# Optimization experiments

Measured on AMD Instinct MI355X. Metric: run time of the kernel, lower is better.

Reference implementation:

```python
import jax, jax.numpy as jnp
import numpy as np

N = 50000        # nodes
E = 200000       # edges
D_IN = 128       # dim_input
D_E = 32         # dim_edge_features
D_H = 256        # dim_hidden
D_OUT = 256      # dim_output
N_LAYERS = 3
N_FRAG = 10000
N_GRAPH = 2000
BN_EPS = 1e-5
GINE_EPS = 0.0   # eps buffer, train_eps=False

_LAYER_DIMS = [(D_IN, D_H), (D_H, D_H), (D_H, D_OUT)]  # (node in, node out) per layer


def setup_inputs() -> dict:
    key = jax.random.key(0)
    ks = iter(jax.random.split(key, 64))
    inp = {}
    inp['x'] = jax.random.normal(next(ks), (N, D_IN), dtype=jnp.float32)
    inp['edge_attr'] = jax.random.normal(next(ks), (E, D_E), dtype=jnp.float32)
    inp['edge_index'] = jax.random.randint(next(ks), (2, E), 0, N, dtype=jnp.int64)
    inp['frag_batch'] = jnp.sort(jax.random.randint(next(ks), (N,), 0, N_FRAG, dtype=jnp.int64))
    inp['graph_batch'] = jnp.sort(jax.random.randint(next(ks), (N,), 0, N_GRAPH, dtype=jnp.int64))
    for i, (din, dout) in enumerate(_LAYER_DIMS):
        fin = din + D_E  # MLP input = node feat + edge feat (post-concat message)
        inp[f'w1_{i}'] = jax.random.normal(next(ks), (fin, D_H), dtype=jnp.float32) / np.sqrt(fin)
        inp[f'b1_{i}'] = jnp.zeros((D_H,), dtype=jnp.float32)
        inp[f'w2_{i}'] = jax.random.normal(next(ks), (D_H, dout), dtype=jnp.float32) / np.sqrt(D_H)
        inp[f'b2_{i}'] = jnp.zeros((dout,), dtype=jnp.float32)
        inp[f'g_{i}'] = jnp.ones((dout,), dtype=jnp.float32)     # BN weight
        inp[f'beta_{i}'] = jnp.zeros((dout,), dtype=jnp.float32)  # BN bias
    return inp


def _gine_layer(x, edge_attr, src, dst, w1, b1, w2, b2, g, beta):
    # message: relu(concat(x_j, e_ji)) gathered along edges  -> [E, din+De]
    m = jax.nn.relu(jnp.concatenate([x[src], edge_attr], axis=-1))
    # aggregate: scatter-add into target nodes -> [N, din+De]
    agg = jax.ops.segment_sum(m, dst, num_segments=N)
    # (1+eps)*x residual on the node-feature slice
    agg = agg.at[:, : x.shape[1]].add((1.0 + GINE_EPS) * x)
    # h_Theta MLP: Linear -> ReLU -> Linear
    h = jnp.dot(jax.nn.relu(jnp.dot(agg, w1) + b1), w2) + b2
    # ReLU then BatchNorm1d(track_running_stats=False): batch stats, biased var
    h = jax.nn.relu(h)
    mu = h.mean(axis=0)
    var = h.var(axis=0)
    return g * (h - mu) * jax.lax.rsqrt(var + BN_EPS) + beta


def _sqrt_pool(h, batch, num_segments):
    # nodes_per_graph, broadcast back per-node, sqrt-normalize, then add-pool
    cnt = jax.ops.segment_sum(jnp.ones((h.shape[0],), h.dtype), batch, num_segments=num_segments)
    inv_sqrt = jax.lax.rsqrt(jnp.maximum(cnt, 1.0))[batch]  # [N]
    return jax.ops.segment_sum(h * inv_sqrt[:, None], batch, num_segments=num_segments)


def reference(x, edge_attr, edge_index, frag_batch, graph_batch,
              w1_0, b1_0, w2_0, b2_0, g_0, beta_0,
              w1_1, b1_1, w2_1, b2_1, g_1, beta_1,
              w1_2, b1_2, w2_2, b2_2, g_2, beta_2):
    src, dst = edge_index[0], edge_index[1]
    params = [(w1_0, b1_0, w2_0, b2_0, g_0, beta_0),
              (w1_1, b1_1, w2_1, b2_1, g_1, beta_1),
              (w1_2, b1_2, w2_2, b2_2, g_2, beta_2)]
    h = x
    for p in params:
        h = _gine_layer(h, edge_attr, src, dst, *p)
    frag_out = _sqrt_pool(h, frag_batch, N_FRAG)    # [N_FRAG, D_OUT]
    graph_out = _sqrt_pool(h, graph_batch, N_GRAPH)  # [N_GRAPH, D_OUT]
    return (frag_out, graph_out)
```

## Files before the change

### kernel.cpp

```cpp
#include <hip/hip_runtime.h>

#define N_NODES 50000
#define N_EDGES 200000
#define DE 32
#define N_FRAG 10000
#define N_GRAPH 2000
#define BN_SLOTS 32
#define KSTR 296

typedef _Float16 f16x8 __attribute__((ext_vector_type(8)));
typedef _Float16 f16x4 __attribute__((ext_vector_type(4)));
typedef __attribute__((ext_vector_type(4))) float f32x4;

__device__ __forceinline__ float4 ld4(const float* p) { return *(const float4*)p; }
__device__ __forceinline__ float4 ld4(const _Float16* p) {
    f16x4 h = *(const f16x4*)p;
    float4 v; v.x = (float)h[0]; v.y = (float)h[1]; v.z = (float)h[2]; v.w = (float)h[3];
    return v;
}
__device__ __forceinline__ void st4h(_Float16* p, float4 v) {
    f16x4 h = {(_Float16)v.x, (_Float16)v.y, (_Float16)v.z, (_Float16)v.w};
    *(f16x4*)p = h;
}

__global__ __launch_bounds__(256)
void count_deg_kernel(const int* __restrict__ ei, int* __restrict__ deg) {
    int e = blockIdx.x * 256 + threadIdx.x;
    if (e < N_EDGES) atomicAdd(&deg[ei[N_EDGES + e]], 1);
}

__global__ __launch_bounds__(256)
void block_sum_kernel(const int* __restrict__ deg, int* __restrict__ bsum) {
    int i = blockIdx.x * 256 + threadIdx.x;
    int v = (i < N_NODES) ? deg[i] : 0;
#pragma unroll
    for (int o = 1; o < 64; o <<= 1) v += __shfl_xor(v, o);
    __shared__ int wsum[4];
    if ((threadIdx.x & 63) == 0) wsum[threadIdx.x >> 6] = v;
    __syncthreads();
    if (threadIdx.x == 0) bsum[blockIdx.x] = wsum[0] + wsum[1] + wsum[2] + wsum[3];
}

__global__ __launch_bounds__(256)
void top_scan_kernel(int* __restrict__ bsum, int nb) {
    __shared__ int s[256];
    int t = threadIdx.x;
    s[t] = (t < nb) ? bsum[t] : 0;
    __syncthreads();
    for (int o = 1; o < 256; o <<= 1) {
        int v = s[t];
        int a = (t >= o) ? s[t - o] : 0;
        __syncthreads();
        s[t] = v + a;
        __syncthreads();
    }
    if (t < nb) bsum[t] = (t > 0) ? s[t - 1] : 0;
}

__global__ __launch_bounds__(256)
void final_scan_kernel(const int* __restrict__ deg, const int* __restrict__ bsum,
                       int* __restrict__ ptr) {
    __shared__ int s[256];
    int i = blockIdx.x * 256 + threadIdx.x;
    int t = threadIdx.x;
    int v = (i < N_NODES) ? deg[i] : 0;
    s[t] = v;
    __syncthreads();
    for (int o = 1; o < 256; o <<= 1) {
        int x = s[t];
        int a = (t >= o) ? s[t - o] : 0;
        __syncthreads();
        s[t] = x + a;
        __syncthreads();
    }
    int incl = s[t];
    int base = bsum[blockIdx.x];
    if (i < N_NODES) ptr[i] = base + incl - v;
    if (i == N_NODES - 1) ptr[N_NODES] = base + incl;
}

__global__ __launch_bounds__(256)
void fill_csr_kernel(const int* __restrict__ ei, const int* __restrict__ row_ptr,
                     int* __restrict__ fill, int* __restrict__ csr_src,
                     int* __restrict__ csr_eid) {
    int e = blockIdx.x * 256 + threadIdx.x;
    if (e >= N_EDGES) return;
    int dst = ei[N_EDGES + e];
    int pos = row_ptr[dst] + atomicAdd(&fill[dst], 1);
    csr_src[pos] = ei[e];
    csr_eid[pos] = e;
}

__global__ __launch_bounds__(256)
void segptr2_kernel(const int* __restrict__ fb, const int* __restrict__ gb,
                    int* __restrict__ frag_ptr, int* __restrict__ graph_ptr) {
    int id = blockIdx.x * 256 + threadIdx.x;
    const int* batch;
    int* ptr;
    int s;
    if (id <= N_FRAG) { batch = fb; ptr = frag_ptr; s = id; }
    else if (id <= N_FRAG + 1 + N_GRAPH) { batch = gb; ptr = graph_ptr; s = id - (N_FRAG + 1); }
    else return;
    int lo = 0, hi = N_NODES;
    while (lo < hi) {
        int mid = (lo + hi) >> 1;
        if (batch[mid] < s) lo = mid + 1; else hi = mid;
    }
    ptr[s] = lo;
}

struct BsAll {
    const float* W[6];
    _Float16* BS[6];
    int base[7];
};

__global__ __launch_bounds__(256)
void bs16_all_kernel(BsAll a) {
    int id = blockIdx.x * 256 + threadIdx.x;
    if (id >= a.base[6]) return;
    int seg = 0;
#pragma unroll
    for (int i = 1; i < 6; ++i) seg += (id >= a.base[i]);
    int lid = id - a.base[seg];
    int j  = lid & 7;
    int l  = (lid >> 3) & 63;
    int cg = (lid >> 9) & 15;
    int kt = lid >> 13;
    int col = cg * 16 + (l & 15);
    int k   = kt * 32 + (l >> 4) * 8 + j;
    a.BS[seg][lid] = (_Float16)a.W[seg][(size_t)k * 256 + col];
}

__global__ __launch_bounds__(256)
void edge_gather_kernel(const float* __restrict__ ea, const int* __restrict__ row_ptr,
                        const int* __restrict__ csr_eid, float* __restrict__ agg_e) {
    int t = threadIdx.x;
    int g = t >> 3;
    int j = t & 7;
    int n = blockIdx.x * 32 + g;
    if (n >= N_NODES) return;
    int col = j << 2;
    float4 acc = {0.f, 0.f, 0.f, 0.f};
    int beg = row_ptr[n], end = row_ptr[n + 1];
    int e = beg;
    float4 va, vb;
    if (e < end) va = *(const float4*)(ea + (size_t)csr_eid[e] * DE + col);
    while (e + 2 <= end) {
        vb = *(const float4*)(ea + (size_t)csr_eid[e + 1] * DE + col);
        acc.x += fmaxf(va.x, 0.f); acc.y += fmaxf(va.y, 0.f);
        acc.z += fmaxf(va.z, 0.f); acc.w += fmaxf(va.w, 0.f);
        if (e + 2 < end) va = *(const float4*)(ea + (size_t)csr_eid[e + 2] * DE + col);
        acc.x += fmaxf(vb.x, 0.f); acc.y += fmaxf(vb.y, 0.f);
        acc.z += fmaxf(vb.z, 0.f); acc.w += fmaxf(vb.w, 0.f);
        e += 2;
    }
    if (e < end) {
        acc.x += fmaxf(va.x, 0.f); acc.y += fmaxf(va.y, 0.f);
        acc.z += fmaxf(va.z, 0.f); acc.w += fmaxf(va.w, 0.f);
    }
    *(float4*)(agg_e + (size_t)n * DE + col) = acc;
}

__global__ __launch_bounds__(256)
void relu16_f32_kernel(const float* __restrict__ x, _Float16* __restrict__ y) {
    size_t i = (size_t)(blockIdx.x * 256 + threadIdx.x) * 4;
    if (i >= (size_t)N_NODES * 128) return;
    float4 v = ld4(x + i);
    f16x4 o = {(_Float16)fmaxf(v.x, 0.f), (_Float16)fmaxf(v.y, 0.f),
               (_Float16)fmaxf(v.z, 0.f), (_Float16)fmaxf(v.w, 0.f)};
    *(f16x4*)(y + i) = o;
}

__global__ __launch_bounds__(256)
void bnfin_relu16_kernel(const float* __restrict__ slots,
                         const float* __restrict__ g, const float* __restrict__ beta,
                         const _Float16* __restrict__ h, _Float16* __restrict__ y,
                         float* __restrict__ scale_out, float* __restrict__ shift_out) {
    __shared__ float ssc[256], ssh[256];
    const int t = threadIdx.x;
    {
        float s = 0.f, q = 0.f;
        for (int k = 0; k < BN_SLOTS; ++k) {
            s += slots[(size_t)k * 512 + t];
            q += slots[(size_t)k * 512 + 256 + t];
        }
        float mu = s * (1.0f / N_NODES);
        float var = q * (1.0f / N_NODES) - mu * mu;
        float rstd = rsqrtf(var + 1e-5f);
        float sc = g[t] * rstd;
        float sh = beta[t] - mu * sc;
        ssc[t] = sc; ssh[t] = sh;
        if (blockIdx.x == 0) { scale_out[t] = sc; shift_out[t] = sh; }
    }
    __syncthreads();
    const size_t total = (size_t)N_NODES * 256 / 8;
    for (size_t idx = (size_t)blockIdx.x * 256 + t; idx < total;
         idx += (size_t)gridDim.x * 256) {
        size_t i = idx * 8;
        int col = (int)(i & 255);
        f16x8 v = *(const f16x8*)(h + i);
        f16x8 o;
#pragma unroll
        for (int k2 = 0; k2 < 8; ++k2)
            o[k2] = (_Float16)fmaxf(fmaf((float)v[k2], ssc[col + k2], ssh[col + k2]), 0.f);
        *(f16x8*)(y + i) = o;
    }
}

template <bool BNIN, typename T, int NC>
__global__ __launch_bounds__(512, 4)
void fused_mlp_kernel(const T* __restrict__ X, const _Float16* __restrict__ Yg,
                      const int* __restrict__ row_ptr, const int* __restrict__ csr_src,
                      const float* __restrict__ agg_e,
                      const float* __restrict__ bnsc, const float* __restrict__ bnsh,
                      const _Float16* __restrict__ B1, const float* __restrict__ bias1,
                      const _Float16* __restrict__ B2, const float* __restrict__ bias2,
                      _Float16* __restrict__ C, float* __restrict__ bnslot) {
    constexpr int DIN  = NC * 32;
    constexpr int K1   = DIN + 32;
    constexpr int NKT1 = K1 / 32;
    constexpr int CPT  = DIN / 8;
    constexpr int NV   = CPT / 8;
    __shared__ __align__(16) _Float16 sBuf[64 * KSTR];
    const int t = threadIdx.x;
    const int l = t & 63;
    const int w = t >> 6;
    const int lr = l & 15;
    const int lq = l >> 4;
    const int row0 = blockIdx.x << 6;
    const int cb = w << 5;

    {
        const int r = t >> 3, j = t & 7;
        const int jc = j << 3;
        const int gr = row0 + r;
        if (gr < N_NODES) {
            f16x8 acc16[NV];
#pragma unroll
            for (int c = 0; c < NV; ++c) acc16[c] = (f16x8){0, 0, 0, 0, 0, 0, 0, 0};
            const int beg = row_ptr[gr], end = row_ptr[gr + 1];
            int e = beg;
            f16x8 va[NV], vb[NV];
            if (e < end) {
                const _Float16* sp = Yg + (size_t)csr_src[e] * DIN + jc;
#pragma unroll
                for (int c = 0; c < NV; ++c) va[c] = *(const f16x8*)(sp + c * 64);
            }
            while (e + 2 <= end) {
                {
                    const _Float16* sp = Yg + (size_t)csr_src[e + 1] * DIN + jc;
#pragma unroll
                    for (int c = 0; c < NV; ++c) vb[c] = *(const f16x8*)(sp + c * 64);
                }
#pragma unroll
                for (int c = 0; c < NV; ++c) acc16[c] += va[c];
                if (e + 2 < end) {
                    const _Float16* sp = Yg + (size_t)csr_src[e + 2] * DIN + jc;
#pragma unroll
                    for (int c = 0; c < NV; ++c) va[c] = *(const f16x8*)(sp + c * 64);
                }
#pragma unroll
                for (int c = 0; c < NV; ++c) acc16[c] += vb[c];
                e += 2;
            }
            if (e < end) {
#pragma unroll
                for (int c = 0; c < NV; ++c) acc16[c] += va[c];
            }
            const T* xp = X + (size_t)gr * DIN + jc;
#pragma unroll
            for (int c = 0; c < NV; ++c) {
                float4 v0f = ld4(xp + c * 64);
                float4 v1f = ld4(xp + c * 64 + 4);
                if (BNIN) {
                    float4 sa = *(const float4*)(bnsc + c * 64 + jc);
                    float4 sb = *(const float4*)(bnsc + c * 64 + jc + 4);
                    float4 ta = *(const float4*)(bnsh + c * 64 + jc);
                    float4 tb = *(const float4*)(bnsh + c * 64 + jc + 4);
                    v0f.x = fmaf(v0f.x, sa.x, ta.x);
                    v0f.y = fmaf(v0f.y, sa.y, ta.y);
                    v0f.z = fmaf(v0f.z, sa.z, ta.z);
                    v0f.w = fmaf(v0f.w, sa.w, ta.w);
                    v1f.x = fmaf(v1f.x, sb.x, tb.x);
                    v1f.y = fmaf(v1f.y, sb.y, tb.y);
                    v1f.z = fmaf(v1f.z, sb.z, tb.z);
                    v1f.w = fmaf(v1f.w, sb.w, tb.w);
                }
                f16x8 o;
                o[0] = (_Float16)(v0f.x + (float)acc16[c][0]);
                o[1] = (_Float16)(v0f.y + (float)acc16[c][1]);
                o[2] = (_Float16)(v0f.z + (float)acc16[c][2]);
                o[3] = (_Float16)(v0f.w + (float)acc16[c][3]);
                o[4] = (_Float16)(v1f.x + (float)acc16[c][4]);
                o[5] = (_Float16)(v1f.y + (float)acc16[c][5]);
                o[6] = (_Float16)(v1f.z + (float)acc16[c][6]);
                o[7] = (_Float16)(v1f.w + (float)acc16[c][7]);
                *(f16x8*)&sBuf[r * KSTR + c * 64 + jc] = o;
            }
            float4 ev = *(const float4*)(agg_e + (size_t)gr * DE + (j << 2));
            st4h(&sBuf[r * KSTR + DIN + (j << 2)], ev);
        } else {
            f16x8 z8 = {0, 0, 0, 0, 0, 0, 0, 0};
#pragma unroll
            for (int c = 0; c < NV; ++c)
                *(f16x8*)&sBuf[r * KSTR + c * 64 + jc] = z8;
            f16x4 z4 = {0, 0, 0, 0};
            *(f16x4*)&sBuf[r * KSTR + DIN + (j << 2)] = z4;
        }
    }
    __syncthreads();

    f32x4 acc1[4][2];
#pragma unroll
    for (int mt = 0; mt < 4; ++mt)
#pragma unroll
        for (int nt = 0; nt < 2; ++nt) acc1[mt][nt] = (f32x4){0.f, 0.f, 0.f, 0.f};
#pragma unroll
    for (int kt = 0; kt < NKT1; ++kt) {
        f16x8 af[4], bf[2];
#pragma unroll
        for (int mt = 0; mt < 4; ++mt)
            af[mt] = *(const f16x8*)&sBuf[(mt * 16 + lr) * KSTR + (kt << 5) + (lq << 3)];
        const size_t bb = ((size_t)(kt * 16 + (w << 1))) * 512 + (l << 3);
#pragma unroll
        for (int nt = 0; nt < 2; ++nt)
            bf[nt] = *(const f16x8*)(B1 + bb + nt * 512);
#pragma unroll
        for (int mt = 0; mt < 4; ++mt)
#pragma unroll
            for (int nt = 0; nt < 2; ++nt)
                acc1[mt][nt] = __builtin_amdgcn_mfma_f32_16x16x32_f16(
                    af[mt], bf[nt], acc1[mt][nt], 0, 0, 0);
    }
    __syncthreads();

#pragma unroll
    for (int nt = 0; nt < 2; ++nt) {
        int col = cb + nt * 16 + lr;
        float bv = bias1[col];
#pragma unroll
        for (int mt = 0; mt < 4; ++mt)
#pragma unroll
            for (int i = 0; i < 4; ++i) {
                int rr = mt * 16 + lq * 4 + i;
                sBuf[rr * KSTR + col] = (_Float16)fmaxf(acc1[mt][nt][i] + bv, 0.f);
            }
    }
    __syncthreads();

    f32x4 acc2[4][2];
#pragma unroll
    for (int mt = 0; mt < 4; ++mt)
#pragma unroll
        for (int nt = 0; nt < 2; ++nt) acc2[mt][nt] = (f32x4){0.f, 0.f, 0.f, 0.f};
#pragma unroll
    for (int kt = 0; kt < 8; ++kt) {
        f16x8 af[4], bf[2];
#pragma unroll
        for (int mt = 0; mt < 4; ++mt)
            af[mt] = *(const f16x8*)&sBuf[(mt * 16 + lr) * KSTR + (kt << 5) + (lq << 3)];
        const size_t bb = ((size_t)(kt * 16 + (w << 1))) * 512 + (l << 3);
#pragma unroll
        for (int nt = 0; nt < 2; ++nt)
            bf[nt] = *(const f16x8*)(B2 + bb + nt * 512);
#pragma unroll
        for (int mt = 0; mt < 4; ++mt)
#pragma unroll
            for (int nt = 0; nt < 2; ++nt)
                acc2[mt][nt] = __builtin_amdgcn_mfma_f32_16x16x32_f16(
                    af[mt], bf[nt], acc2[mt][nt], 0, 0, 0);
    }
    __syncthreads();

    float* slot = bnslot + (size_t)(blockIdx.x & (BN_SLOTS - 1)) * 512;
#pragma unroll
    for (int nt = 0; nt < 2; ++nt) {
        int col = cb + nt * 16 + lr;
        float bv = bias2[col];
        float s = 0.f, qq = 0.f;
#pragma unroll
        for (int mt = 0; mt < 4; ++mt)
#pragma unroll
            for (int i = 0; i < 4; ++i) {
                int rr = mt * 16 + lq * 4 + i;
                float o = fmaxf(acc2[mt][nt][i] + bv, 0.f);
                sBuf[rr * KSTR + col] = (_Float16)o;
                if (row0 + rr < N_NODES) { s += o; qq += o * o; }
            }
        s += __shfl_xor(s, 16); s += __shfl_xor(s, 32);
        qq += __shfl_xor(qq, 16); qq += __shfl_xor(qq, 32);
        if (lq == 0) {
            atomicAdd(&slot[col], s);
            atomicAdd(&slot[256 + col], qq);
        }
    }
    __syncthreads();

#pragma unroll
    for (int k = 0; k < 4; ++k) {
        int rr  = (t >> 5) + k * 16;
        int col = (t & 31) * 8;
        int row = row0 + rr;
        if (row < N_NODES) {
            f16x8 v = *(const f16x8*)&sBuf[rr * KSTR + col];
            *(f16x8*)(C + (size_t)row * 256 + col) = v;
        }
    }
}

__global__ void bn_finalize_kernel(const float* __restrict__ slots,
                                   const float* __restrict__ g, const float* __restrict__ beta,
                                   float* __restrict__ scale, float* __restrict__ shift) {
    int c = threadIdx.x;
    float s = 0.f, q = 0.f;
    for (int k = 0; k < BN_SLOTS; ++k) {
        s += slots[(size_t)k * 512 + c];
        q += slots[(size_t)k * 512 + 256 + c];
    }
    float mu = s * (1.0f / N_NODES);
    float var = q * (1.0f / N_NODES) - mu * mu;
    float rstd = rsqrtf(var + 1e-5f);
    float sc = g[c] * rstd;
    scale[c] = sc;
    shift[c] = beta[c] - mu * sc;
}

__global__ __launch_bounds__(256)
void pool_both_kernel(const _Float16* __restrict__ h,
                      const int* __restrict__ frag_ptr, const int* __restrict__ graph_ptr,
                      const float* __restrict__ bnsc, const float* __restrict__ bnsh,
                      float* __restrict__ out) {
    const int NFB = (N_FRAG + 3) / 4;
    int b = blockIdx.x;
    const int* ptr; float* o; int nseg; int sb;
    if (b < NFB) { ptr = frag_ptr; o = out; nseg = N_FRAG; sb = b * 4; }
    else { ptr = graph_ptr; o = out + (size_t)N_FRAG * 256; nseg = N_GRAPH; sb = (b - NFB) * 4; }
    int t = threadIdx.x;
    int g = t >> 6;
    int j = t & 63;
    int s = sb + g;
    if (s >= nseg) return;
    int beg = ptr[s], end = ptr[s + 1];
    int col = j << 2;
    float4 sc = *(const float4*)(bnsc + col);
    float4 sh = *(const float4*)(bnsh + col);
    float4 acc = {0.f, 0.f, 0.f, 0.f};
    for (int i = beg; i < end; ++i) {
        float4 v = ld4(h + (size_t)i * 256 + col);
        acc.x += fmaf(v.x, sc.x, sh.x);
        acc.y += fmaf(v.y, sc.y, sh.y);
        acc.z += fmaf(v.z, sc.z, sh.z);
        acc.w += fmaf(v.w, sc.w, sh.w);
    }
    float w = rsqrtf(fmaxf((float)(end - beg), 1.0f));
    float4 ov = {acc.x * w, acc.y * w, acc.z * w, acc.w * w};
    *(float4*)(o + (size_t)s * 256 + col) = ov;
}

extern "C" void kernel_launch(void* const* d_in, const int* in_sizes, int n_in,
                              void* d_out, int out_size, void* d_ws, size_t ws_size,
                              hipStream_t stream) {
    const float* x  = (const float*)d_in[0];
    const float* ea = (const float*)d_in[1];
    const int*   ei = (const int*)d_in[2];
    const int*   fb = (const int*)d_in[3];
    const int*   gb = (const int*)d_in[4];
    const float* W1[3]   = {(const float*)d_in[5],  (const float*)d_in[11], (const float*)d_in[17]};
    const float* B1[3]   = {(const float*)d_in[6],  (const float*)d_in[12], (const float*)d_in[18]};
    const float* W2[3]   = {(const float*)d_in[7],  (const float*)d_in[13], (const float*)d_in[19]};
    const float* B2[3]   = {(const float*)d_in[8],  (const float*)d_in[14], (const float*)d_in[20]};
    const float* G[3]    = {(const float*)d_in[9],  (const float*)d_in[15], (const float*)d_in[21]};
    const float* BETA[3] = {(const float*)d_in[10], (const float*)d_in[16], (const float*)d_in[22]};

    const int FIN[3] = {160, 288, 288};
    const int NBLK = (N_NODES + 255) / 256;

    float* ws = (float*)d_ws;
    size_t off = 0;
    _Float16* bufA = (_Float16*)(ws + off); off += (size_t)N_NODES * 128;
    _Float16* bufB = (_Float16*)(ws + off); off += (size_t)N_NODES * 128;
    _Float16* ybuf = (_Float16*)(ws + off); off += (size_t)N_NODES * 128;
    float* agg_e = ws + off; off += (size_t)N_NODES * DE;
    float* bnss  = ws + off; off += 3 * 512;
    float* bnslots = ws + off; off += (size_t)3 * BN_SLOTS * 512;
    _Float16* w1f[3]; _Float16* w2f[3];
    {
        _Float16* sw = (_Float16*)(ws + off);
        _Float16* sw0 = sw;
        for (int l = 0; l < 3; ++l) { w1f[l] = sw; sw += 256 * FIN[l]; }
        for (int l = 0; l < 3; ++l) { w2f[l] = sw; sw += 256 * 256; }
        off += (size_t)(sw - sw0 + 1) / 2;
    }
    int* iw      = (int*)(ws + off);
    int* row_ptr = iw;                     iw += N_NODES + 1;
    int* deg     = iw;                     iw += N_NODES;
    int* fill    = iw;                     iw += N_NODES;
    int* csr_src = iw;                     iw += N_EDGES;
    int* csr_eid = iw;                     iw += N_EDGES;
    int* frag_ptr = iw;                    iw += N_FRAG + 1;
    int* graph_ptr = iw;                   iw += N_GRAPH + 1;
    int* bsum    = iw;                     iw += NBLK;

    hipMemsetAsync(deg, 0, 2 * N_NODES * sizeof(int), stream);
    hipMemsetAsync(bnslots, 0, (size_t)3 * BN_SLOTS * 512 * sizeof(float), stream);

    {
        BsAll a;
        a.W[0] = W1[0]; a.W[1] = W1[1]; a.W[2] = W1[2];
        a.W[3] = W2[0]; a.W[4] = W2[1]; a.W[5] = W2[2];
        a.BS[0] = w1f[0]; a.BS[1] = w1f[1]; a.BS[2] = w1f[2];
        a.BS[3] = w2f[0]; a.BS[4] = w2f[1]; a.BS[5] = w2f[2];
        int Ks[6] = {FIN[0], FIN[1], FIN[2], 256, 256, 256};
        int cum = 0;
        for (int i = 0; i < 6; ++i) { a.base[i] = cum; cum += Ks[i] * 256; }
        a.base[6] = cum;
        bs16_all_kernel<<<(cum + 255) / 256, 256, 0, stream>>>(a);
    }

    count_deg_kernel<<<(N_EDGES + 255) / 256, 256, 0, stream>>>(ei, deg);
    block_sum_kernel<<<NBLK, 256, 0, stream>>>(deg, bsum);
    top_scan_kernel<<<1, 256, 0, stream>>>(bsum, NBLK);
    final_scan_kernel<<<NBLK, 256, 0, stream>>>(deg, bsum, row_ptr);
    fill_csr_kernel<<<(N_EDGES + 255) / 256, 256, 0, stream>>>(ei, row_ptr, fill, csr_src, csr_eid);

    segptr2_kernel<<<(N_FRAG + N_GRAPH + 2 + 255) / 256, 256, 0, stream>>>(
        fb, gb, frag_ptr, graph_ptr);

    edge_gather_kernel<<<(N_NODES + 31) / 32, 256, 0, stream>>>(ea, row_ptr, csr_eid, agg_e);

    const int nblk_mlp = (N_NODES + 63) / 64;
    relu16_f32_kernel<<<(N_NODES * 128 / 4 + 255) / 256, 256, 0, stream>>>(x, ybuf);
    fused_mlp_kernel<false, float, 4><<<nblk_mlp, 512, 0, stream>>>(
        x, ybuf, row_ptr, csr_src, agg_e, nullptr, nullptr,
        w1f[0], B1[0], w2f[0], B2[0], bufA, bnslots);

    bnfin_relu16_kernel<<<1024, 256, 0, stream>>>(
        bnslots, G[0], BETA[0], bufA, ybuf, bnss, bnss + 256);
    fused_mlp_kernel<true, _Float16, 8><<<nblk_mlp, 512, 0, stream>>>(
        bufA, ybuf, row_ptr, csr_src, agg_e, bnss, bnss + 256,
        w1f[1], B1[1], w2f[1], B2[1], bufB, bnslots + (size_t)1 * BN_SLOTS * 512);

    bnfin_relu16_kernel<<<1024, 256, 0, stream>>>(
        bnslots + (size_t)1 * BN_SLOTS * 512, G[1], BETA[1], bufB, ybuf,
        bnss + 512, bnss + 768);
    fused_mlp_kernel<true, _Float16, 8><<<nblk_mlp, 512, 0, stream>>>(
        bufB, ybuf, row_ptr, csr_src, agg_e, bnss + 512, bnss + 768,
        w1f[2], B1[2], w2f[2], B2[2], bufA, bnslots + (size_t)2 * BN_SLOTS * 512);

    bn_finalize_kernel<<<1, 256, 0, stream>>>(
        bnslots + (size_t)2 * BN_SLOTS * 512, G[2], BETA[2], bnss + 1024, bnss + 1280);
    const int NFB = (N_FRAG + 3) / 4, NGB = (N_GRAPH + 3) / 4;
    pool_both_kernel<<<NFB + NGB, 256, 0, stream>>>(
        bufA, frag_ptr, graph_ptr, bnss + 1024, bnss + 1280, (float*)d_out);
}
```

Measured before the change: 349.1 us.

## Merge prep kernels, fuse edge gather into first MLP, fold BN finalize into pool

The weight conversion, degree count, segment-pointer search and input ReLU conversion now run as one launch, with each block picking its task by block index. The edge-feature aggregation moves into the first fused MLP layer, which also writes agg_e for later layers, so one standalone gather kernel goes away. The last BN finalize is recomputed in every pool block instead of running as a single-block kernel. The double-buffered prefetch in the neighbour gather loop becomes a simple loop, bnfin grid sizes are halved, and the result is fewer launches in exchange for less memory-level parallelism in the gather and redundant per-block BN work.

New measurement: 335.2 us. 1.04x faster.

```diff
diff --git a/kernel.cpp b/kernel.cpp
--- a/kernel.cpp
+++ b/kernel.cpp
@@ -21,12 +21,6 @@
 __device__ __forceinline__ void st4h(_Float16* p, float4 v) {
     f16x4 h = {(_Float16)v.x, (_Float16)v.y, (_Float16)v.z, (_Float16)v.w};
     *(f16x4*)p = h;
-}
-
-__global__ __launch_bounds__(256)
-void count_deg_kernel(const int* __restrict__ ei, int* __restrict__ deg) {
-    int e = blockIdx.x * 256 + threadIdx.x;
-    if (e < N_EDGES) atomicAdd(&deg[ei[N_EDGES + e]], 1);
 }
 
 __global__ __launch_bounds__(256)
@@ -91,85 +85,73 @@
     csr_eid[pos] = e;
 }
 
-__global__ __launch_bounds__(256)
-void segptr2_kernel(const int* __restrict__ fb, const int* __restrict__ gb,
-                    int* __restrict__ frag_ptr, int* __restrict__ graph_ptr) {
-    int id = blockIdx.x * 256 + threadIdx.x;
-    const int* batch;
-    int* ptr;
-    int s;
-    if (id <= N_FRAG) { batch = fb; ptr = frag_ptr; s = id; }
-    else if (id <= N_FRAG + 1 + N_GRAPH) { batch = gb; ptr = graph_ptr; s = id - (N_FRAG + 1); }
-    else return;
-    int lo = 0, hi = N_NODES;
-    while (lo < hi) {
-        int mid = (lo + hi) >> 1;
-        if (batch[mid] < s) lo = mid + 1; else hi = mid;
-    }
-    ptr[s] = lo;
-}
-
-struct BsAll {
+struct PrepArgs {
     const float* W[6];
     _Float16* BS[6];
     int base[7];
+    int nb_bs;
+    const int* ei;
+    int* deg;
+    int nb_deg;
+    const int* fb; const int* gb;
+    int* frag_ptr; int* graph_ptr;
+    int nb_seg;
+    const float* x;
+    _Float16* y0;
 };
 
 __global__ __launch_bounds__(256)
-void bs16_all_kernel(BsAll a) {
-    int id = blockIdx.x * 256 + threadIdx.x;
-    if (id >= a.base[6]) return;
-    int seg = 0;
-#pragma unroll
-    for (int i = 1; i < 6; ++i) seg += (id >= a.base[i]);
-    int lid = id - a.base[seg];
-    int j  = lid & 7;
-    int l  = (lid >> 3) & 63;
-    int cg = (lid >> 9) & 15;
-    int kt = lid >> 13;
-    int col = cg * 16 + (l & 15);
-    int k   = kt * 32 + (l >> 4) * 8 + j;
-    a.BS[seg][lid] = (_Float16)a.W[seg][(size_t)k * 256 + col];
-}
-
-__global__ __launch_bounds__(256)
-void edge_gather_kernel(const float* __restrict__ ea, const int* __restrict__ row_ptr,
-                        const int* __restrict__ csr_eid, float* __restrict__ agg_e) {
-    int t = threadIdx.x;
-    int g = t >> 3;
-    int j = t & 7;
-    int n = blockIdx.x * 32 + g;
-    if (n >= N_NODES) return;
-    int col = j << 2;
-    float4 acc = {0.f, 0.f, 0.f, 0.f};
-    int beg = row_ptr[n], end = row_ptr[n + 1];
-    int e = beg;
-    float4 va, vb;
-    if (e < end) va = *(const float4*)(ea + (size_t)csr_eid[e] * DE + col);
-    while (e + 2 <= end) {
-        vb = *(const float4*)(ea + (size_t)csr_eid[e + 1] * DE + col);
-        acc.x += fmaxf(va.x, 0.f); acc.y += fmaxf(va.y, 0.f);
-        acc.z += fmaxf(va.z, 0.f); acc.w += fmaxf(va.w, 0.f);
-        if (e + 2 < end) va = *(const float4*)(ea + (size_t)csr_eid[e + 2] * DE + col);
-        acc.x += fmaxf(vb.x, 0.f); acc.y += fmaxf(vb.y, 0.f);
-        acc.z += fmaxf(vb.z, 0.f); acc.w += fmaxf(vb.w, 0.f);
-        e += 2;
-    }
-    if (e < end) {
-        acc.x += fmaxf(va.x, 0.f); acc.y += fmaxf(va.y, 0.f);
-        acc.z += fmaxf(va.z, 0.f); acc.w += fmaxf(va.w, 0.f);
-    }
-    *(float4*)(agg_e + (size_t)n * DE + col) = acc;
-}
-
-__global__ __launch_bounds__(256)
-void relu16_f32_kernel(const float* __restrict__ x, _Float16* __restrict__ y) {
-    size_t i = (size_t)(blockIdx.x * 256 + threadIdx.x) * 4;
-    if (i >= (size_t)N_NODES * 128) return;
-    float4 v = ld4(x + i);
-    f16x4 o = {(_Float16)fmaxf(v.x, 0.f), (_Float16)fmaxf(v.y, 0.f),
-               (_Float16)fmaxf(v.z, 0.f), (_Float16)fmaxf(v.w, 0.f)};
-    *(f16x4*)(y + i) = o;
+void prep1_kernel(PrepArgs a) {
+    int b = blockIdx.x;
+    const int t = threadIdx.x;
+    if (b < a.nb_bs) {
+        int id = b * 256 + t;
+        if (id < a.base[6]) {
+            int seg = 0;
+#pragma unroll
+            for (int i = 1; i < 6; ++i) seg += (id >= a.base[i]);
+            int lid = id - a.base[seg];
+            int j  = lid & 7;
+            int l  = (lid >> 3) & 63;
+            int cg = (lid >> 9) & 15;
+            int kt = lid >> 13;
+            int col = cg * 16 + (l & 15);
+            int k   = kt * 32 + (l >> 4) * 8 + j;
+            a.BS[seg][lid] = (_Float16)a.W[seg][(size_t)k * 256 + col];
+        }
+        return;
+    }
+    b -= a.nb_bs;
+    if (b < a.nb_deg) {
+        int e = b * 256 + t;
+        if (e < N_EDGES) atomicAdd(&a.deg[a.ei[N_EDGES + e]], 1);
+        return;
+    }
+    b -= a.nb_deg;
+    if (b < a.nb_seg) {
+        int id = b * 256 + t;
+        const int* batch;
+        int* ptr;
+        int s;
+        if (id <= N_FRAG) { batch = a.fb; ptr = a.frag_ptr; s = id; }
+        else if (id <= N_FRAG + 1 + N_GRAPH) { batch = a.gb; ptr = a.graph_ptr; s = id - (N_FRAG + 1); }
+        else return;
+        int lo = 0, hi = N_NODES;
+        while (lo < hi) {
+            int mid = (lo + hi) >> 1;
+            if (batch[mid] < s) lo = mid + 1; else hi = mid;
+        }
+        ptr[s] = lo;
+        return;
+    }
+    b -= a.nb_seg;
+    size_t i = ((size_t)b * 256 + t) * 4;
+    if (i < (size_t)N_NODES * 128) {
+        float4 v = ld4(a.x + i);
+        f16x4 o = {(_Float16)fmaxf(v.x, 0.f), (_Float16)fmaxf(v.y, 0.f),
+                   (_Float16)fmaxf(v.z, 0.f), (_Float16)fmaxf(v.w, 0.f)};
+        *(f16x4*)(a.y0 + i) = o;
+    }
 }
 
 __global__ __launch_bounds__(256)
@@ -212,7 +194,8 @@
 __global__ __launch_bounds__(512, 4)
 void fused_mlp_kernel(const T* __restrict__ X, const _Float16* __restrict__ Yg,
                       const int* __restrict__ row_ptr, const int* __restrict__ csr_src,
-                      const float* __restrict__ agg_e,
+                      const int* __restrict__ csr_eid, const float* __restrict__ ea,
+                      float* __restrict__ agg_e,
                       const float* __restrict__ bnsc, const float* __restrict__ bnsh,
                       const _Float16* __restrict__ B1, const float* __restrict__ bias1,
                       const _Float16* __restrict__ B2, const float* __restrict__ bias2,
@@ -239,34 +222,19 @@
             f16x8 acc16[NV];
 #pragma unroll
             for (int c = 0; c < NV; ++c) acc16[c] = (f16x8){0, 0, 0, 0, 0, 0, 0, 0};
+            float4 eacc = {0.f, 0.f, 0.f, 0.f};
             const int beg = row_ptr[gr], end = row_ptr[gr + 1];
-            int e = beg;
-            f16x8 va[NV], vb[NV];
-            if (e < end) {
+            for (int e = beg; e < end; ++e) {
                 const _Float16* sp = Yg + (size_t)csr_src[e] * DIN + jc;
 #pragma unroll
-                for (int c = 0; c < NV; ++c) va[c] = *(const f16x8*)(sp + c * 64);
-            }
-            while (e + 2 <= end) {
-                {
-                    const _Float16* sp = Yg + (size_t)csr_src[e + 1] * DIN + jc;
-#pragma unroll
-                    for (int c = 0; c < NV; ++c) vb[c] = *(const f16x8*)(sp + c * 64);
+                for (int c = 0; c < NV; ++c) acc16[c] += *(const f16x8*)(sp + c * 64);
+                if (!BNIN) {
+                    float4 ev = *(const float4*)(ea + (size_t)csr_eid[e] * DE + (j << 2));
+                    eacc.x += fmaxf(ev.x, 0.f);
+                    eacc.y += fmaxf(ev.y, 0.f);
+                    eacc.z += fmaxf(ev.z, 0.f);
+                    eacc.w += fmaxf(ev.w, 0.f);
                 }
-#pragma unroll
-                for (int c = 0; c < NV; ++c) acc16[c] += va[c];
-                if (e + 2 < end) {
-                    const _Float16* sp = Yg + (size_t)csr_src[e + 2] * DIN + jc;
-#pragma unroll
-                    for (int c = 0; c < NV; ++c) va[c] = *(const f16x8*)(sp + c * 64);
-                }
-#pragma unroll
-                for (int c = 0; c < NV; ++c) acc16[c] += vb[c];
-                e += 2;
-            }
-            if (e < end) {
-#pragma unroll
-                for (int c = 0; c < NV; ++c) acc16[c] += va[c];
             }
             const T* xp = X + (size_t)gr * DIN + jc;
 #pragma unroll
@@ -298,8 +266,13 @@
                 o[7] = (_Float16)(v1f.w + (float)acc16[c][7]);
                 *(f16x8*)&sBuf[r * KSTR + c * 64 + jc] = o;
             }
-            float4 ev = *(const float4*)(agg_e + (size_t)gr * DE + (j << 2));
-            st4h(&sBuf[r * KSTR + DIN + (j << 2)], ev);
+            if (!BNIN) {
+                *(float4*)(agg_e + (size_t)gr * DE + (j << 2)) = eacc;
+                st4h(&sBuf[r * KSTR + DIN + (j << 2)], eacc);
+            } else {
+                float4 ev = *(const float4*)(agg_e + (size_t)gr * DE + (j << 2));
+                st4h(&sBuf[r * KSTR + DIN + (j << 2)], ev);
+            }
         } else {
             f16x8 z8 = {0, 0, 0, 0, 0, 0, 0, 0};
 #pragma unroll
@@ -409,42 +382,41 @@
     }
 }
 
-__global__ void bn_finalize_kernel(const float* __restrict__ slots,
-                                   const float* __restrict__ g, const float* __restrict__ beta,
-                                   float* __restrict__ scale, float* __restrict__ shift) {
-    int c = threadIdx.x;
-    float s = 0.f, q = 0.f;
-    for (int k = 0; k < BN_SLOTS; ++k) {
-        s += slots[(size_t)k * 512 + c];
-        q += slots[(size_t)k * 512 + 256 + c];
-    }
-    float mu = s * (1.0f / N_NODES);
-    float var = q * (1.0f / N_NODES) - mu * mu;
-    float rstd = rsqrtf(var + 1e-5f);
-    float sc = g[c] * rstd;
-    scale[c] = sc;
-    shift[c] = beta[c] - mu * sc;
-}
-
 __global__ __launch_bounds__(256)
 void pool_both_kernel(const _Float16* __restrict__ h,
                       const int* __restrict__ frag_ptr, const int* __restrict__ graph_ptr,
-                      const float* __restrict__ bnsc, const float* __restrict__ bnsh,
+                      const float* __restrict__ slots,
+                      const float* __restrict__ g2, const float* __restrict__ beta2,
                       float* __restrict__ out) {
+    __shared__ float ssc[256], ssh[256];
+    const int t = threadIdx.x;
+    {
+        float s = 0.f, q = 0.f;
+        for (int k = 0; k < BN_SLOTS; ++k) {
+            s += slots[(size_t)k * 512 + t];
+            q += slots[(size_t)k * 512 + 256 + t];
+        }
+        float mu = s * (1.0f / N_NODES);
+        float var = q * (1.0f / N_NODES) - mu * mu;
+        float rstd = rsqrtf(var + 1e-5f);
+        float sc = g2[t] * rstd;
+        ssc[t] = sc;
+        ssh[t] = beta2[t] - mu * sc;
+    }
+    __syncthreads();
     const int NFB = (N_FRAG + 3) / 4;
     int b = blockIdx.x;
     const int* ptr; float* o; int nseg; int sb;
     if (b < NFB) { ptr = frag_ptr; o = out; nseg = N_FRAG; sb = b * 4; }
     else { ptr = graph_ptr; o = out + (size_t)N_FRAG * 256; nseg = N_GRAPH; sb = (b - NFB) * 4; }
-    int t = threadIdx.x;
     int g = t >> 6;
     int j = t & 63;
     int s = sb + g;
     if (s >= nseg) return;
     int beg = ptr[s], end = ptr[s + 1];
     int col = j << 2;
-    float4 sc = *(const float4*)(bnsc + col);
-    float4 sh = *(const float4*)(bnsh + col);
+    float4 sc = *(const float4*)(ssc + col);
+    float4 sh = *(const float4*)(ssh + col);
     float4 acc = {0.f, 0.f, 0.f, 0.f};
     for (int i = beg; i < end; ++i) {
         float4 v = ld4(h + (size_t)i * 256 + col);
@@ -506,7 +478,7 @@
     hipMemsetAsync(bnslots, 0, (size_t)3 * BN_SLOTS * 512 * sizeof(float), stream);
 
     {
-        BsAll a;
+        PrepArgs a;
         a.W[0] = W1[0]; a.W[1] = W1[1]; a.W[2] = W1[2];
         a.W[3] = W2[0]; a.W[4] = W2[1]; a.W[5] = W2[2];
         a.BS[0] = w1f[0]; a.BS[1] = w1f[1]; a.BS[2] = w1f[2];
@@ -515,42 +487,41 @@
         int cum = 0;
         for (int i = 0; i < 6; ++i) { a.base[i] = cum; cum += Ks[i] * 256; }
         a.base[6] = cum;
-        bs16_all_kernel<<<(cum + 255) / 256, 256, 0, stream>>>(a);
-    }
-
-    count_deg_kernel<<<(N_EDGES + 255) / 256, 256, 0, stream>>>(ei, deg);
+        a.nb_bs  = (cum + 255) / 256;
+        a.ei = ei; a.deg = deg;
+        a.nb_deg = (N_EDGES + 255) / 256;
+        a.fb = fb; a.gb = gb; a.frag_ptr = frag_ptr; a.graph_ptr = graph_ptr;
+        a.nb_seg = (N_FRAG + N_GRAPH + 2 + 255) / 256;
+        a.x = x; a.y0 = ybuf;
+        int nb_relu = (N_NODES * 128 / 4 + 255) / 256;
+        prep1_kernel<<<a.nb_bs + a.nb_deg + a.nb_seg + nb_relu, 256, 0, stream>>>(a);
+    }
+
     block_sum_kernel<<<NBLK, 256, 0, stream>>>(deg, bsum);
     top_scan_kernel<<<1, 256, 0, stream>>>(bsum, NBLK);
     final_scan_kernel<<<NBLK, 256, 0, stream>>>(deg, bsum, row_ptr);
     fill_csr_kernel<<<(N_EDGES + 255) / 256, 256, 0, stream>>>(ei, row_ptr, fill, csr_src, csr_eid);
 
-    segptr2_kernel<<<(N_FRAG + N_GRAPH + 2 + 255) / 256, 256, 0, stream>>>(
-        fb, gb, frag_ptr, graph_ptr);
-
-    edge_gather_kernel<<<(N_NODES + 31) / 32, 256, 0, stream>>>(ea, row_ptr, csr_eid, agg_e);
-
     const int nblk_mlp = (N_NODES + 63) / 64;
-    relu16_f32_kernel<<<(N_NODES * 128 / 4 + 255) / 256, 256, 0, stream>>>(x, ybuf);
     fused_mlp_kernel<false, float, 4><<<nblk_mlp, 512, 0, stream>>>(
-        x, ybuf, row_ptr, csr_src, agg_e, nullptr, nullptr,
+        x, ybuf, row_ptr, csr_src, csr_eid, ea, agg_e, nullptr, nullptr,
         w1f[0], B1[0], w2f[0], B2[0], bufA, bnslots);
 
-    bnfin_relu16_kernel<<<1024, 256, 0, stream>>>(
+    bnfin_relu16_kernel<<<512, 256, 0, stream>>>(
         bnslots, G[0], BETA[0], bufA, ybuf, bnss, bnss + 256);
     fused_mlp_kernel<true, _Float16, 8><<<nblk_mlp, 512, 0, stream>>>(
-        bufA, ybuf, row_ptr, csr_src, agg_e, bnss, bnss + 256,
+        bufA, ybuf, row_ptr, csr_src, nullptr, nullptr, agg_e, bnss, bnss + 256,
         w1f[1], B1[1], w2f[1], B2[1], bufB, bnslots + (size_t)1 * BN_SLOTS * 512);
 
-    bnfin_relu16_kernel<<<1024, 256, 0, stream>>>(
+    bnfin_relu16_kernel<<<512, 256, 0, stream>>>(
         bnslots + (size_t)1 * BN_SLOTS * 512, G[1], BETA[1], bufB, ybuf,
         bnss + 512, bnss + 768);
     fused_mlp_kernel<true, _Float16, 8><<<nblk_mlp, 512, 0, stream>>>(
-        bufB, ybuf, row_ptr, csr_src, agg_e, bnss + 512, bnss + 768,
+        bufB, ybuf, row_ptr, csr_src, nullptr, nullptr, agg_e, bnss + 512, bnss + 768,
         w1f[2], B1[2], w2f[2], B2[2], bufA, bnslots + (size_t)2 * BN_SLOTS * 512);
 
-    bn_finalize_kernel<<<1, 256, 0, stream>>>(
-        bnslots + (size_t)2 * BN_SLOTS * 512, G[2], BETA[2], bnss + 1024, bnss + 1280);
     const int NFB = (N_FRAG + 3) / 4, NGB = (N_GRAPH + 3) / 4;
     pool_both_kernel<<<NFB + NGB, 256, 0, stream>>>(
-        bufA, frag_ptr, graph_ptr, bnss + 1024, bnss + 1280, (float*)d_out);
-}
+        bufA, frag_ptr, graph_ptr, bnslots + (size_t)2 * BN_SLOTS * 512,
+        G[2], BETA[2], (float*)d_out);
+}
```
